# Kernel tuning notes

Measured on AMD Instinct MI355X. Metric: run time of the kernel, lower is better.

The kernel has to match this reference:

```python
import jax, jax.numpy as jnp
import numpy as np

PI = float(np.pi)
EPS = 1e-8

N, M, K, D = 20000, 20000, 32, 64
HID, OUT = 64, 192
PPF_OUT = OUT // 3  # 64


def safe_atan2(y, x):
    x_safe = jnp.where(jnp.abs(x) < EPS, jnp.sign(x) * EPS, x)
    return jnp.arctan2(y, x_safe)


def _angle(a, b):
    # a, b: [N, K, 3] -> normalized angle in [0,1]: atan2(|a x b|, a.b)/pi
    y = jnp.sum(a * b, axis=-1, keepdims=True)
    x = jnp.cross(a, b, axis=-1)
    x_norm = jnp.linalg.norm(x, axis=-1, keepdims=True)
    return safe_atan2(x_norm, y) / PI


def calc_ppf(points, point_normals, neighbor_points, neighbor_normals):
    # points [N,3], point_normals [N,3], neighbor_* [N,K,3]
    p = points[:, None, :]
    pn = jnp.broadcast_to(point_normals[:, None, :], neighbor_points.shape)
    vec_d = neighbor_points - p
    d = jnp.linalg.norm(vec_d, axis=-1, keepdims=True)
    angle1 = _angle(pn, vec_d)
    angle2 = _angle(neighbor_normals, vec_d)
    angle3 = _angle(pn, neighbor_normals)
    return jnp.concatenate([d, angle1, angle2, angle3], axis=-1)  # [N,K,4]


def setup_inputs() -> dict:
    key = jax.random.key(0)
    ks = jax.random.split(key, 16)
    inp = {
        "q_pts": jax.random.normal(ks[0], (N, 3), jnp.float32),
        "s_pts": jax.random.normal(ks[1], (M, 3), jnp.float32),
        "s_feats": jax.random.normal(ks[2], (M, D, 3), jnp.float32),
        "neighbor_indices": jax.random.randint(ks[3], (N, K), 0, M, jnp.int32),
        "normals": jax.random.normal(ks[4], (M, 3), jnp.float32),
        # ppf_encoder: Linear(4,HID) -> ReLU -> Linear(HID,HID) -> ReLU -> Linear(HID,PPF_OUT)
        "W1": jax.random.normal(ks[5], (HID, 4), jnp.float32) * 0.5,
        "b1": jnp.zeros((HID,), jnp.float32),
        "W2": jax.random.normal(ks[6], (HID, HID), jnp.float32) * 0.125,
        "b2": jnp.zeros((HID,), jnp.float32),
        "W3": jax.random.normal(ks[7], (PPF_OUT, HID), jnp.float32) * 0.125,
        "b3": jnp.zeros((PPF_OUT,), jnp.float32),
        # gate_proj: Linear(PPF_OUT, OUT)
        "Wg": jax.random.normal(ks[8], (OUT, PPF_OUT), jnp.float32) * 0.125,
        "bg": jnp.zeros((OUT,), jnp.float32),
        # vn_value: VNLinear(D, OUT) -> weight [OUT, D], no bias
        "Wv": jax.random.normal(ks[9], (OUT, D), jnp.float32) * 0.125,
    }
    return inp


def reference(q_pts, s_pts, s_feats, neighbor_indices, normals,
              W1, b1, W2, b2, W3, b3, Wg, bg, Wv):
    # gather neighbors
    neighbor_pts = s_pts[neighbor_indices]        # [N,K,3]
    neighbor_norms = normals[neighbor_indices]    # [N,K,3]
    q_normals = normals[neighbor_indices[:, 0]]   # [N,3]

    ppf = calc_ppf(q_pts, q_normals, neighbor_pts, neighbor_norms)  # [N,K,4]

    h = jax.nn.relu(ppf @ W1.T + b1)
    h = jax.nn.relu(h @ W2.T + b2)
    ppf_encoded = h @ W3.T + b3                   # [N,K,PPF_OUT]
    ppf_mod = jnp.mean(ppf_encoded, axis=1)       # [N,PPF_OUT]
    gate = jax.nn.sigmoid(ppf_mod @ Wg.T + bg)    # [N,OUT]

    neighbor_feats = s_feats[neighbor_indices]    # [N,K,D,3]
    aggregated = jnp.mean(neighbor_feats, axis=1) # [N,D,3]
    transformed = jnp.einsum('od,ndt->not', Wv, aggregated)  # [N,OUT,3]

    return transformed * gate[:, :, None]
```

## Files before the change

kernel.cpp:

```cpp
#include <hip/hip_runtime.h>
#include <hip/hip_bf16.h>
#include <math.h>

#define NPTS 20000
#define KNB  32
#define DDIM 64
#define HIDN 64
#define OUTC 192
#define PPB  4

#define WS_W2 0
#define WS_W3 4096
#define WS_W1 8192
#define WS_WG 10240
#define WS_WV 22528

typedef short bf16x8 __attribute__((ext_vector_type(8)));
typedef float f32x4  __attribute__((ext_vector_type(4)));

union BF8 { bf16x8 v; unsigned short us[8]; unsigned u[4]; };

__device__ __forceinline__ unsigned short f2bf(float f) {
  return __builtin_bit_cast(unsigned short, __float2bfloat16(f));
}

__device__ __forceinline__ float fast_atan2pi(float y, float x) {
  const float ax = fabsf(x);
  const float mx = fmaxf(fmaxf(ax, y), 1e-30f);
  const float mn = fminf(ax, y);
  const float t  = mn * __builtin_amdgcn_rcpf(mx);
  const float s  = t * t;
  float p = -0.0117212f;
  p = fmaf(p, s,  0.05265332f);
  p = fmaf(p, s, -0.11643287f);
  p = fmaf(p, s,  0.19354346f);
  p = fmaf(p, s, -0.33262347f);
  p = fmaf(p, s,  0.99997726f);
  float r = p * t;
  if (y > ax)  r = 1.5707963268f - r;
  if (x < 0.f) r = 3.1415926536f - r;
  return r * 0.3183098862f;
}

__device__ __forceinline__ float angle3f(float ax, float ay, float az,
                                         float bx, float by, float bz) {
  const float y  = ax*bx + ay*by + az*bz;
  const float cx = ay*bz - az*by;
  const float cy = az*bx - ax*bz;
  const float cz = ax*by - ay*bx;
  const float xn = __builtin_amdgcn_sqrtf(cx*cx + cy*cy + cz*cz);
  return fast_atan2pi(xn, y);
}

__global__ void prep_weights(const float* __restrict__ W1, const float* __restrict__ W2,
                             const float* __restrict__ W3, const float* __restrict__ Wg,
                             const float* __restrict__ Wv, unsigned short* __restrict__ ws)
{
  const int f  = blockIdx.x;
  const int L  = threadIdx.x;
  const int ln = L & 15, lq = L >> 4;
  unsigned short vals[8];
  if (f >= 16 && f < 20) {
    const int ct = f - 16;
#pragma unroll
    for (int j = 0; j < 8; ++j) {
      const float v = (lq == 0 && j < 4) ? W1[(ln + 16*ct)*4 + j] : 0.f;
      vals[j] = f2bf(v);
    }
  } else {
    const float* M; int q;
    if (f < 8)       { M = W2; q = f; }
    else if (f < 16) { M = W3; q = f - 8; }
    else if (f < 44) { M = Wg; q = f - 20; }
    else             { M = Wv; q = f - 44; }
    const int ct = q >> 1, ks = q & 1;
    const float* src = M + (ln + 16*ct)*64 + lq*8 + 32*ks;
#pragma unroll
    for (int j = 0; j < 8; ++j) vals[j] = f2bf(src[j]);
  }
  uint4 w;
  w.x = vals[0] | ((unsigned)vals[1] << 16);
  w.y = vals[2] | ((unsigned)vals[3] << 16);
  w.z = vals[4] | ((unsigned)vals[5] << 16);
  w.w = vals[6] | ((unsigned)vals[7] << 16);
  *(uint4*)&ws[f*512 + L*8] = w;
}

__global__ __launch_bounds__(256, 4)
void ppf_fused(const float* __restrict__ q_pts,
               const float* __restrict__ s_pts,
               const float* __restrict__ s_feats,
               const int*   __restrict__ nbr,
               const float* __restrict__ normals,
               const float* __restrict__ b1, const float* __restrict__ b2,
               const float* __restrict__ b3, const float* __restrict__ bg,
               const unsigned short* __restrict__ wsu,
               float* __restrict__ out)
{
  __shared__ __align__(16) unsigned short s_h[PPB][KNB][72];
  __shared__ __align__(16) float s_ppf[PPB][KNB][4];
  __shared__ __align__(16) unsigned short s_modb[16][72];
  __shared__ __align__(16) unsigned short s_aggb[16][72];
  __shared__ float s_gate[PPB][200];
  float* s_out = (float*)&s_h[0][0][0];

  const int tid  = threadIdx.x;
  const int g    = tid >> 6;
  const int lane = tid & 63;
  const int lq   = lane >> 4;
  const int ln   = lane & 15;
  const int pu   = __builtin_amdgcn_readfirstlane(blockIdx.x * PPB + g);

  {
    const float qx = q_pts[pu*3+0], qy = q_pts[pu*3+1], qz = q_pts[pu*3+2];
    const int   i0 = nbr[pu*KNB];
    const float qnx = normals[i0*3+0], qny = normals[i0*3+1], qnz = normals[i0*3+2];
    const int k  = lane & 31;
    const int mi = nbr[pu*KNB + k];
    const float px = s_pts[mi*3+0], py = s_pts[mi*3+1], pz = s_pts[mi*3+2];
    const float nx = normals[mi*3+0], ny = normals[mi*3+1], nz = normals[mi*3+2];
    const float vx = px - qx, vy = py - qy, vz = pz - qz;
    if (lane < KNB) {
      s_ppf[g][k][1] = angle3f(qnx,qny,qnz, vx,vy,vz);
      s_ppf[g][k][2] = angle3f(nx,ny,nz,    vx,vy,vz);
    } else {
      s_ppf[g][k][0] = __builtin_amdgcn_sqrtf(vx*vx + vy*vy + vz*vz);
      s_ppf[g][k][3] = angle3f(qnx,qny,qnz, nx,ny,nz);
    }
  }

  {
    BF8 a1[2];
    a1[0].u[0]=a1[0].u[1]=a1[0].u[2]=a1[0].u[3]=0;
    a1[1] = a1[0];
    if (lq == 0) {
#pragma unroll
      for (int rt = 0; rt < 2; ++rt) {
        const float4 pv = *(const float4*)&s_ppf[g][ln + 16*rt][0];
        a1[rt].us[0]=f2bf(pv.x); a1[rt].us[1]=f2bf(pv.y);
        a1[rt].us[2]=f2bf(pv.z); a1[rt].us[3]=f2bf(pv.w);
      }
    }
#pragma unroll
    for (int ct = 0; ct < 4; ++ct) {
      const bf16x8 bw = *(const bf16x8*)&wsu[WS_W1 + ct*512 + lane*8];
      const float  bv = b1[ln + 16*ct];
#pragma unroll
      for (int rt = 0; rt < 2; ++rt) {
        f32x4 c = {bv, bv, bv, bv};
        c = __builtin_amdgcn_mfma_f32_16x16x32_bf16(a1[rt].v, bw, c, 0, 0, 0);
#pragma unroll
        for (int r = 0; r < 4; ++r)
          s_h[g][lq*4 + r + 16*rt][ln + 16*ct] = f2bf(fmaxf(c[r], 0.f));
      }
    }
  }

  {
    bf16x8 wf[8];
#pragma unroll
    for (int fIdx = 0; fIdx < 8; ++fIdx)
      wf[fIdx] = *(const bf16x8*)&wsu[WS_W2 + fIdx*512 + lane*8];
    bf16x8 a2[4];
#pragma unroll
    for (int rt = 0; rt < 2; ++rt)
#pragma unroll
      for (int ks = 0; ks < 2; ++ks)
        a2[rt*2+ks] = *(const bf16x8*)&s_h[g][ln + 16*rt][lq*8 + ks*32];
#pragma unroll
    for (int ct = 0; ct < 4; ++ct) {
      const float bv = b2[ln + 16*ct];
#pragma unroll
      for (int rt = 0; rt < 2; ++rt) {
        f32x4 c = {bv, bv, bv, bv};
        c = __builtin_amdgcn_mfma_f32_16x16x32_bf16(a2[rt*2+0], wf[ct*2+0], c, 0, 0, 0);
        c = __builtin_amdgcn_mfma_f32_16x16x32_bf16(a2[rt*2+1], wf[ct*2+1], c, 0, 0, 0);
#pragma unroll
        for (int r = 0; r < 4; ++r)
          s_h[g][lq*4 + r + 16*rt][ln + 16*ct] = f2bf(fmaxf(c[r], 0.f));
      }
    }
  }

  {
    bf16x8 wf[8];
#pragma unroll
    for (int fIdx = 0; fIdx < 8; ++fIdx)
      wf[fIdx] = *(const bf16x8*)&wsu[WS_W3 + fIdx*512 + lane*8];
    bf16x8 a3[4];
#pragma unroll
    for (int rt = 0; rt < 2; ++rt)
#pragma unroll
      for (int ks = 0; ks < 2; ++ks)
        a3[rt*2+ks] = *(const bf16x8*)&s_h[g][ln + 16*rt][lq*8 + ks*32];
#pragma unroll
    for (int ct = 0; ct < 4; ++ct) {
      const float bv = b3[ln + 16*ct];
      f32x4 c0 = {bv, bv, bv, bv};
      c0 = __builtin_amdgcn_mfma_f32_16x16x32_bf16(a3[0], wf[ct*2+0], c0, 0, 0, 0);
      c0 = __builtin_amdgcn_mfma_f32_16x16x32_bf16(a3[1], wf[ct*2+1], c0, 0, 0, 0);
      f32x4 c1 = {bv, bv, bv, bv};
      c1 = __builtin_amdgcn_mfma_f32_16x16x32_bf16(a3[2], wf[ct*2+0], c1, 0, 0, 0);
      c1 = __builtin_amdgcn_mfma_f32_16x16x32_bf16(a3[3], wf[ct*2+1], c1, 0, 0, 0);
      float s = (c0[0]+c0[1]+c0[2]+c0[3]) + (c1[0]+c1[1]+c1[2]+c1[3]);
      s += __shfl_xor(s, 16);
      s += __shfl_xor(s, 32);
      if (lq == 0) s_modb[g][ln + 16*ct] = f2bf(s * (1.f/KNB));
    }
  }

  {
    float s0 = 0.f, s1 = 0.f, s2 = 0.f;
    const int lofs = lane * 3;
#pragma unroll 8
    for (int k = 0; k < KNB; ++k) {
      const int mi = nbr[pu*KNB + k];
      const float* fr = s_feats + (size_t)mi*(DDIM*3) + lofs;
      s0 += fr[0]; s1 += fr[1]; s2 += fr[2];
    }
    s_aggb[g*3+0][lane] = f2bf(s0 * (1.f/KNB));
    s_aggb[g*3+1][lane] = f2bf(s1 * (1.f/KNB));
    s_aggb[g*3+2][lane] = f2bf(s2 * (1.f/KNB));
  }
  __syncthreads();

  {
    const bf16x8 am0 = *(const bf16x8*)&s_modb[ln][lq*8];
    const bf16x8 am1 = *(const bf16x8*)&s_modb[ln][lq*8 + 32];
#pragma unroll
    for (int t = 0; t < 3; ++t) {
      const int ot = g*3 + t;
      const bf16x8 bg0 = *(const bf16x8*)&wsu[WS_WG + (ot*2+0)*512 + lane*8];
      const bf16x8 bg1 = *(const bf16x8*)&wsu[WS_WG + (ot*2+1)*512 + lane*8];
      const float  bv  = bg[ln + 16*ot];
      f32x4 c = {bv, bv, bv, bv};
      c = __builtin_amdgcn_mfma_f32_16x16x32_bf16(am0, bg0, c, 0, 0, 0);
      c = __builtin_amdgcn_mfma_f32_16x16x32_bf16(am1, bg1, c, 0, 0, 0);
      if (lq == 0) {
#pragma unroll
        for (int r = 0; r < 4; ++r)
          s_gate[r][ln + 16*ot] = 1.f / (1.f + __expf(-c[r]));
      }
    }
  }

  {
    const bf16x8 ab0 = *(const bf16x8*)&s_aggb[ln][lq*8];
    const bf16x8 ab1 = *(const bf16x8*)&s_aggb[ln][lq*8 + 32];
    const int gi = ln / 3;
    const int tt = ln - gi*3;
#pragma unroll
    for (int t2 = 0; t2 < 3; ++t2) {
      const int ot = g*3 + t2;
      const bf16x8 av0 = *(const bf16x8*)&wsu[WS_WV + (ot*2+0)*512 + lane*8];
      const bf16x8 av1 = *(const bf16x8*)&wsu[WS_WV + (ot*2+1)*512 + lane*8];
      f32x4 c = {0.f, 0.f, 0.f, 0.f};
      c = __builtin_amdgcn_mfma_f32_16x16x32_bf16(av0, ab0, c, 0, 0, 0);
      c = __builtin_amdgcn_mfma_f32_16x16x32_bf16(av1, ab1, c, 0, 0, 0);
      if (ln < 12) {
#pragma unroll
        for (int r = 0; r < 4; ++r) {
          const int o = 16*ot + lq*4 + r;
          s_out[gi*592 + o*3 + tt] = c[r] * s_gate[gi][o];
        }
      }
    }
  }
  __syncthreads();

  {
    float4* outv = (float4*)out;
    const float4* sov = (const float4*)s_out;
#pragma unroll
    for (int i = 0; i < 3; ++i) {
      const int idx = tid + 256*i;
      if (idx < 576) {
        const int gg  = idx / 144;
        const int off = idx - gg*144;
        outv[(size_t)blockIdx.x * 576 + idx] = sov[gg*148 + off];
      }
    }
  }
}

extern "C" void kernel_launch(void* const* d_in, const int* in_sizes, int n_in,
                              void* d_out, int out_size, void* d_ws, size_t ws_size,
                              hipStream_t stream) {
  const float* q_pts   = (const float*)d_in[0];
  const float* s_pts   = (const float*)d_in[1];
  const float* s_feats = (const float*)d_in[2];
  const int*   nbr     = (const int*)  d_in[3];
  const float* normals = (const float*)d_in[4];
  const float* W1 = (const float*)d_in[5];
  const float* b1 = (const float*)d_in[6];
  const float* W2 = (const float*)d_in[7];
  const float* b2 = (const float*)d_in[8];
  const float* W3 = (const float*)d_in[9];
  const float* b3 = (const float*)d_in[10];
  const float* Wg = (const float*)d_in[11];
  const float* bg = (const float*)d_in[12];
  const float* Wv = (const float*)d_in[13];
  float* out = (float*)d_out;
  unsigned short* ws = (unsigned short*)d_ws;

  hipLaunchKernelGGL(prep_weights, dim3(68), dim3(64), 0, stream,
                     W1, W2, W3, Wg, Wv, ws);
  hipLaunchKernelGGL(ppf_fused, dim3(NPTS / PPB), dim3(256), 0, stream,
                     q_pts, s_pts, s_feats, nbr, normals,
                     b1, b2, b3, bg, ws, out);
}
```

Baseline: 171.4 us.

## Software-pipeline s_feats neighbor gather across the MLP stages

```diff
diff --git a/kernel.cpp b/kernel.cpp
--- a/kernel.cpp
+++ b/kernel.cpp
@@ -86,7 +86,24 @@
   *(uint4*)&ws[f*512 + L*8] = w;
 }
 
-__global__ __launch_bounds__(256, 4)
+__device__ __forceinline__ void gather_issue(const float* __restrict__ s_feats,
+                                             const int* __restrict__ nbr,
+                                             int pu, int base, int lofs,
+                                             float3* __restrict__ buf) {
+#pragma unroll
+  for (int k = 0; k < 8; ++k) {
+    const int mi = nbr[pu*KNB + base + k];
+    const float* fr = s_feats + (size_t)mi*(DDIM*3) + lofs;
+    buf[k] = make_float3(fr[0], fr[1], fr[2]);
+  }
+}
+__device__ __forceinline__ void gather_acc(const float3* __restrict__ buf,
+                                           float& s0, float& s1, float& s2) {
+#pragma unroll
+  for (int k = 0; k < 8; ++k) { s0 += buf[k].x; s1 += buf[k].y; s2 += buf[k].z; }
+}
+
+__global__ __launch_bounds__(256, 5)
 void ppf_fused(const float* __restrict__ q_pts,
                const float* __restrict__ s_pts,
                const float* __restrict__ s_feats,
@@ -98,7 +115,6 @@
                float* __restrict__ out)
 {
   __shared__ __align__(16) unsigned short s_h[PPB][KNB][72];
-  __shared__ __align__(16) float s_ppf[PPB][KNB][4];
   __shared__ __align__(16) unsigned short s_modb[16][72];
   __shared__ __align__(16) unsigned short s_aggb[16][72];
   __shared__ float s_gate[PPB][200];
@@ -110,6 +126,12 @@
   const int lq   = lane >> 4;
   const int ln   = lane & 15;
   const int pu   = __builtin_amdgcn_readfirstlane(blockIdx.x * PPB + g);
+  const int lofs = lane * 3;
+
+  float3 bufA[8], bufB[8];
+  float s0 = 0.f, s1 = 0.f, s2 = 0.f;
+
+  gather_issue(s_feats, nbr, pu, 0, lofs, bufA);
 
   {
     const float qx = q_pts[pu*3+0], qy = q_pts[pu*3+1], qz = q_pts[pu*3+2];
@@ -120,12 +142,13 @@
     const float px = s_pts[mi*3+0], py = s_pts[mi*3+1], pz = s_pts[mi*3+2];
     const float nx = normals[mi*3+0], ny = normals[mi*3+1], nz = normals[mi*3+2];
     const float vx = px - qx, vy = py - qy, vz = pz - qz;
+    float* ppfrow = (float*)&s_h[g][k][64];
     if (lane < KNB) {
-      s_ppf[g][k][1] = angle3f(qnx,qny,qnz, vx,vy,vz);
-      s_ppf[g][k][2] = angle3f(nx,ny,nz,    vx,vy,vz);
+      ppfrow[1] = angle3f(qnx,qny,qnz, vx,vy,vz);
+      ppfrow[2] = angle3f(nx,ny,nz,    vx,vy,vz);
     } else {
-      s_ppf[g][k][0] = __builtin_amdgcn_sqrtf(vx*vx + vy*vy + vz*vz);
-      s_ppf[g][k][3] = angle3f(qnx,qny,qnz, nx,ny,nz);
+      ppfrow[0] = __builtin_amdgcn_sqrtf(vx*vx + vy*vy + vz*vz);
+      ppfrow[3] = angle3f(qnx,qny,qnz, nx,ny,nz);
     }
   }
 
@@ -136,7 +159,7 @@
     if (lq == 0) {
 #pragma unroll
       for (int rt = 0; rt < 2; ++rt) {
-        const float4 pv = *(const float4*)&s_ppf[g][ln + 16*rt][0];
+        const float4 pv = *(const float4*)&s_h[g][ln + 16*rt][64];
         a1[rt].us[0]=f2bf(pv.x); a1[rt].us[1]=f2bf(pv.y);
         a1[rt].us[2]=f2bf(pv.z); a1[rt].us[3]=f2bf(pv.w);
       }
@@ -155,6 +178,9 @@
       }
     }
   }
+
+  gather_issue(s_feats, nbr, pu, 8, lofs, bufB);
+  gather_acc(bufA, s0, s1, s2);
 
   {
     bf16x8 wf[8];
@@ -181,6 +207,9 @@
       }
     }
   }
+
+  gather_issue(s_feats, nbr, pu, 16, lofs, bufA);
+  gather_acc(bufB, s0, s1, s2);
 
   {
     bf16x8 wf[8];
@@ -209,19 +238,14 @@
     }
   }
 
-  {
-    float s0 = 0.f, s1 = 0.f, s2 = 0.f;
-    const int lofs = lane * 3;
-#pragma unroll 8
-    for (int k = 0; k < KNB; ++k) {
-      const int mi = nbr[pu*KNB + k];
-      const float* fr = s_feats + (size_t)mi*(DDIM*3) + lofs;
-      s0 += fr[0]; s1 += fr[1]; s2 += fr[2];
-    }
-    s_aggb[g*3+0][lane] = f2bf(s0 * (1.f/KNB));
-    s_aggb[g*3+1][lane] = f2bf(s1 * (1.f/KNB));
-    s_aggb[g*3+2][lane] = f2bf(s2 * (1.f/KNB));
-  }
+  gather_issue(s_feats, nbr, pu, 24, lofs, bufB);
+  gather_acc(bufA, s0, s1, s2);
+  gather_acc(bufB, s0, s1, s2);
+
+  s_aggb[g*3+0][lane] = f2bf(s0 * (1.f/KNB));
+  s_aggb[g*3+1][lane] = f2bf(s1 * (1.f/KNB));
+  s_aggb[g*3+2][lane] = f2bf(s2 * (1.f/KNB));
+
   __syncthreads();
 
   {
```

Result: slower. 233.4 us (+36.1%).
